# Kernel tuning notes

Measured on AMD Instinct MI355X. Metric: run time of the kernel, lower is better.

Reference implementation:

```python
import jax, jax.numpy as jnp
import numpy as np

H = 64  # hidden_size
IN = 1  # input_size
OUT = 32  # fc output


def _lstm_layer(x, Wih, Whh, bih, bhh):
    """x: (B,T,D_in). Returns (outputs (B,T,H), final h (B,H)). PyTorch gate order i,f,g,o."""
    B = x.shape[0]
    b = bih + bhh  # (4H,)
    # precompute input contributions for all timesteps: (T,B,4H)
    xW = jnp.einsum('btd,gd->tbg', x, Wih) + b

    def step(carry, xw_t):
        h, c = carry
        gates = xw_t + h @ Whh.T  # (B,4H)
        i, f, g, o = jnp.split(gates, 4, axis=-1)
        i = jax.nn.sigmoid(i)
        f = jax.nn.sigmoid(f)
        g = jnp.tanh(g)
        o = jax.nn.sigmoid(o)
        c = f * c + i * g
        h = o * jnp.tanh(c)
        return (h, c), h

    h0 = jnp.zeros((B, H), dtype=x.dtype)
    c0 = jnp.zeros((B, H), dtype=x.dtype)
    (h_T, _), hs = jax.lax.scan(step, (h0, c0), xW)
    return jnp.swapaxes(hs, 0, 1), h_T


def setup_inputs() -> dict:
    key = jax.random.key(0)
    ks = jax.random.split(key, 11)
    s_ih0 = 1.0 / np.sqrt(H)
    inp = {
        'x': jax.random.normal(ks[0], (2048, 512, IN), dtype=jnp.float32),
        # layer 0: input_size -> H
        'Wih0': jax.random.uniform(ks[1], (4 * H, IN), minval=-s_ih0, maxval=s_ih0),
        'Whh0': jax.random.uniform(ks[2], (4 * H, H), minval=-s_ih0, maxval=s_ih0),
        'bih0': jax.random.uniform(ks[3], (4 * H,), minval=-s_ih0, maxval=s_ih0),
        'bhh0': jax.random.uniform(ks[4], (4 * H,), minval=-s_ih0, maxval=s_ih0),
        # layer 1: H -> H
        'Wih1': jax.random.uniform(ks[5], (4 * H, H), minval=-s_ih0, maxval=s_ih0),
        'Whh1': jax.random.uniform(ks[6], (4 * H, H), minval=-s_ih0, maxval=s_ih0),
        'bih1': jax.random.uniform(ks[7], (4 * H,), minval=-s_ih0, maxval=s_ih0),
        'bhh1': jax.random.uniform(ks[8], (4 * H,), minval=-s_ih0, maxval=s_ih0),
        # fc: H -> 32
        'fcW': jax.random.uniform(ks[9], (OUT, H), minval=-s_ih0, maxval=s_ih0),
        'fcb': jax.random.uniform(ks[10], (OUT,), minval=-s_ih0, maxval=s_ih0),
    }
    return inp


def reference(x, Wih0, Whh0, bih0, bhh0, Wih1, Whh1, bih1, bhh1, fcW, fcb):
    h1_seq, _ = _lstm_layer(x, Wih0, Whh0, bih0, bhh0)
    _, h_last = _lstm_layer(h1_seq, Wih1, Whh1, bih1, bhh1)  # hidden[-1]
    features = jax.nn.relu(h_last @ fcW.T + fcb)  # (B, 32)
    return features
```

## Files before the change

### kernel.cpp

```cpp
#include <hip/hip_runtime.h>
#include <hip/hip_bf16.h>


#define HID 64
#define TSTEPS 512
#define MB 8
#define RS 80

typedef _Float16 f16x8 __attribute__((ext_vector_type(8)));
typedef float f32x4 __attribute__((ext_vector_type(4)));

#define KSIG (-1.44269504089f)
#define KTANH (2.88539008178f)

__device__ __forceinline__ float sig1(float p) {
    return __builtin_amdgcn_rcpf(1.f + __builtin_amdgcn_exp2f(p));
}
__device__ __forceinline__ float th1(float p) {
    return 1.f - 2.f * __builtin_amdgcn_rcpf(1.f + __builtin_amdgcn_exp2f(p));
}

#define MFMA16(A, B, C) __builtin_amdgcn_mfma_f32_16x16x32_f16((A), (B), (C), 0, 0, 0)

__global__ __launch_bounds__(512, 1) void lstm_feat_kernel(
    const float* __restrict__ x,
    const float* __restrict__ Wih0, const float* __restrict__ Whh0,
    const float* __restrict__ bih0, const float* __restrict__ bhh0,
    const float* __restrict__ Wih1, const float* __restrict__ Whh1,
    const float* __restrict__ bih1, const float* __restrict__ bhh1,
    const float* __restrict__ fcW, const float* __restrict__ fcb,
    float* __restrict__ out)
{
    __shared__ __align__(16) float x_lds[(MB / 2) * TSTEPS * 2];
    __shared__ __align__(16) _Float16 h0_lds[4][MB * RS];
    __shared__ __align__(16) _Float16 h1_lds[2][MB * RS];
    __shared__ float h1f32[MB * HID];
    __shared__ float fcw_lds[HID * 32];
    __shared__ float fcb_lds[32];

    const int tid  = threadIdx.x;
    const int wave = tid >> 6;
    const int lane = tid & 63;
    const int nq   = lane & 15;
    const int quad = lane >> 4;
    const int bbase = blockIdx.x * MB;
    const bool isL1 = (wave >= 4);
    const int ug = wave & 3;
    const int u  = ug * 16 + nq;

    for (int i = tid; i < TSTEPS * MB; i += 512) {
        int r = i >> 9, t = i & (TSTEPS - 1);
        x_lds[(r >> 1) * (TSTEPS * 2) + t * 2 + (r & 1)] = x[(bbase + r) * TSTEPS + t];
    }
    for (int i = tid; i < 32 * HID; i += 512) {
        int o = i >> 6, kk = i & 63;
        fcw_lds[kk * 32 + o] = fcW[i];
    }
    if (tid < 32) fcb_lds[tid] = fcb[tid];
    for (int i = tid; i < 4 * MB * RS; i += 512) ((_Float16*)h0_lds)[i] = (_Float16)0.f;
    for (int i = tid; i < 2 * MB * RS; i += 512) ((_Float16*)h1_lds)[i] = (_Float16)0.f;

    f16x8 wA[4][2], wB[4][2];
    f32x4 cbias[4];
    float wx0s[4];
    {
        const float* Wa = isL1 ? Wih1 : Whh0;
        const float* bi = isL1 ? bih1 : bih0;
        const float* bh = isL1 ? bhh1 : bhh0;
        #pragma unroll
        for (int g = 0; g < 4; ++g) {
            const float sc = (g == 2) ? KTANH : KSIG;
            const int n = g * 64 + u;
            const float bs = (bi[n] + bh[n]) * sc;
            cbias[g] = (f32x4){bs, bs, bs, bs};
            wx0s[g] = Wih0[n] * sc;
            #pragma unroll
            for (int ks = 0; ks < 2; ++ks) {
                const int k0 = quad * 8 + ks * 32;
                f16x8 a;
                #pragma unroll
                for (int j = 0; j < 8; ++j)
                    a[j] = (_Float16)(Wa[n * HID + k0 + j] * sc);
                wA[g][ks] = a;
            }
        }
        if (isL1) {
            #pragma unroll
            for (int g = 0; g < 4; ++g) {
                const float sc = (g == 2) ? KTANH : KSIG;
                const int n = g * 64 + u;
                #pragma unroll
                for (int ks = 0; ks < 2; ++ks) {
                    const int k0 = quad * 8 + ks * 32;
                    f16x8 b;
                    #pragma unroll
                    for (int j = 0; j < 8; ++j)
                        b[j] = (_Float16)(Whh1[n * HID + k0 + j] * sc);
                    wB[g][ks] = b;
                }
            }
        }
    }

    const int arow = (nq >> 1) * RS + quad * 8;
    const int b0r  = (quad * 2) * RS;
    const int hbase = quad * 2;
    float c0 = 0.f, c1 = 0.f;
    f32x4 l0ac[4], l1ac[4];

    __syncthreads();

#define L0A(S) do {                                                               \
    f16x8 a0 = *(const f16x8*)&h0_lds[S][arow];                                   \
    f16x8 a1 = *(const f16x8*)&h0_lds[S][arow + 32];                              \
    __builtin_amdgcn_s_setprio(1);                                                \
    _Pragma("unroll")                                                             \
    for (int g = 0; g < 4; ++g) l0ac[g] = MFMA16(a0, wA[g][0], cbias[g]);         \
    _Pragma("unroll")                                                             \
    for (int g = 0; g < 4; ++g) l0ac[g] = MFMA16(a1, wA[g][1], l0ac[g]);          \
    __builtin_amdgcn_s_setprio(0);                                                \
} while (0)

#define L0B(Q, XA, XB) do {                                                       \
    float pi0 = fmaf((XA), wx0s[0], l0ac[0][0]), pi1 = fmaf((XB), wx0s[0], l0ac[0][2]); \
    float pf0 = fmaf((XA), wx0s[1], l0ac[1][0]), pf1 = fmaf((XB), wx0s[1], l0ac[1][2]); \
    float pg0 = fmaf((XA), wx0s[2], l0ac[2][0]), pg1 = fmaf((XB), wx0s[2], l0ac[2][2]); \
    float po0 = fmaf((XA), wx0s[3], l0ac[3][0]), po1 = fmaf((XB), wx0s[3], l0ac[3][2]); \
    float iv0 = sig1(pi0), iv1 = sig1(pi1), fv0 = sig1(pf0), fv1 = sig1(pf1);     \
    float gv0 = th1(pg0),  gv1 = th1(pg1),  ov0 = sig1(po0), ov1 = sig1(po1);     \
    c0 = fmaf(fv0, c0, iv0 * gv0);  c1 = fmaf(fv1, c1, iv1 * gv1);                \
    h0_lds[Q][b0r + u]      = (_Float16)(ov0 * th1(c0 * KTANH));                  \
    h0_lds[Q][b0r + RS + u] = (_Float16)(ov1 * th1(c1 * KTANH));                  \
} while (0)

#define L1A(H1S) do {                                                             \
    float iv0 = sig1(l1ac[0][0]), iv1 = sig1(l1ac[0][2]);                         \
    float fv0 = sig1(l1ac[1][0]), fv1 = sig1(l1ac[1][2]);                         \
    float gv0 = th1(l1ac[2][0]),  gv1 = th1(l1ac[2][2]);                          \
    float ov0 = sig1(l1ac[3][0]), ov1 = sig1(l1ac[3][2]);                         \
    c0 = fmaf(fv0, c0, iv0 * gv0);  c1 = fmaf(fv1, c1, iv1 * gv1);                \
    h1_lds[H1S][b0r + u]      = (_Float16)(ov0 * th1(c0 * KTANH));                \
    h1_lds[H1S][b0r + RS + u] = (_Float16)(ov1 * th1(c1 * KTANH));                \
} while (0)

#define L1B(SH0, H1S) do {                                                        \
    f16x8 a00 = *(const f16x8*)&h0_lds[SH0][arow];                                \
    f16x8 a01 = *(const f16x8*)&h0_lds[SH0][arow + 32];                           \
    f16x8 a10 = *(const f16x8*)&h1_lds[H1S][arow];                                \
    f16x8 a11 = *(const f16x8*)&h1_lds[H1S][arow + 32];                           \
    __builtin_amdgcn_s_setprio(1);                                                \
    _Pragma("unroll")                                                             \
    for (int g = 0; g < 4; ++g) l1ac[g] = MFMA16(a00, wA[g][0], cbias[g]);        \
    _Pragma("unroll")                                                             \
    for (int g = 0; g < 4; ++g) l1ac[g] = MFMA16(a01, wA[g][1], l1ac[g]);         \
    _Pragma("unroll")                                                             \
    for (int g = 0; g < 4; ++g) l1ac[g] = MFMA16(a10, wB[g][0], l1ac[g]);         \
    _Pragma("unroll")                                                             \
    for (int g = 0; g < 4; ++g) l1ac[g] = MFMA16(a11, wB[g][1], l1ac[g]);         \
    __builtin_amdgcn_s_setprio(0);                                                \
} while (0)

#define IV(S, H1S, XA, XB, DOA, DOB) do {                                         \
    if (!isL1) { L0A(S); } else if (DOA) { L1A(H1S); }                            \
    __syncthreads();                                                              \
    if (!isL1) { L0B((S + 1) & 3, XA, XB); } else if (DOB) { L1B((S + 3) & 3, H1S); } \
    __syncthreads();                                                              \
} while (0)

    const int xoff = quad * (TSTEPS * 2);

    {
        const f32x4 xv0 = *(const f32x4*)&x_lds[xoff + 0];
        const f32x4 xv1 = *(const f32x4*)&x_lds[xoff + 4];
        IV(0, 0, xv0[0], xv0[1], false, false);
        IV(1, 1, xv0[2], xv0[3], false, false);
        IV(2, 0, xv1[0], xv1[1], false, true);
        IV(3, 1, xv1[2], xv1[3], true,  true);
    }

    for (int n = 4; n < TSTEPS; n += 4) {
        const f32x4 xv0 = *(const f32x4*)&x_lds[xoff + n * 2];
        const f32x4 xv1 = *(const f32x4*)&x_lds[xoff + n * 2 + 4];
        IV(0, 0, xv0[0], xv0[1], true, true);
        IV(1, 1, xv0[2], xv0[3], true, true);
        IV(2, 0, xv1[0], xv1[1], true, true);
        IV(3, 1, xv1[2], xv1[3], true, true);
    }

    if (isL1) L1A(0);
    __syncthreads();
    if (isL1) L1B(3, 0);
    __syncthreads();
    if (isL1) L1A(1);
    __syncthreads();
    if (isL1) L1B(0, 1);
    __syncthreads();

    if (isL1) {
        float iv0 = sig1(l1ac[0][0]), iv1 = sig1(l1ac[0][2]);
        float fv0 = sig1(l1ac[1][0]), fv1 = sig1(l1ac[1][2]);
        float gv0 = th1(l1ac[2][0]),  gv1 = th1(l1ac[2][2]);
        float ov0 = sig1(l1ac[3][0]), ov1 = sig1(l1ac[3][2]);
        c0 = fmaf(fv0, c0, iv0 * gv0);  c1 = fmaf(fv1, c1, iv1 * gv1);
        h1f32[hbase * HID + u]       = ov0 * th1(c0 * KTANH);
        h1f32[(hbase + 1) * HID + u] = ov1 * th1(c1 * KTANH);
    }
    __syncthreads();

    if (tid < MB * 32) {
        const int o  = tid & 31;
        const int rr = tid >> 5;
        float acc = fcb_lds[o];
        #pragma unroll 8
        for (int kk = 0; kk < HID; ++kk)
            acc += h1f32[rr * HID + kk] * fcw_lds[kk * 32 + o];
        out[(bbase + rr) * 32 + o] = fmaxf(acc, 0.f);
    }
}

extern "C" void kernel_launch(void* const* d_in, const int* in_sizes, int n_in,
                              void* d_out, int out_size, void* d_ws, size_t ws_size,
                              hipStream_t stream) {
    const float* x    = (const float*)d_in[0];
    const float* Wih0 = (const float*)d_in[1];
    const float* Whh0 = (const float*)d_in[2];
    const float* bih0 = (const float*)d_in[3];
    const float* bhh0 = (const float*)d_in[4];
    const float* Wih1 = (const float*)d_in[5];
    const float* Whh1 = (const float*)d_in[6];
    const float* bih1 = (const float*)d_in[7];
    const float* bhh1 = (const float*)d_in[8];
    const float* fcW  = (const float*)d_in[9];
    const float* fcb  = (const float*)d_in[10];
    float* out = (float*)d_out;

    lstm_feat_kernel<<<2048 / MB, 512, 0, stream>>>(
        x, Wih0, Whh0, bih0, bhh0, Wih1, Whh1, bih1, bhh1, fcW, fcb, out);
}
```

Before: 337.8 us.

## Split LSTM gate work across 16 waves and pair gates via lane shuffles

The block grows from 512 to 1024 threads (16 waves). Each wave now covers 8 hidden units, with lanes 0-7 holding the i/g gates and lanes 8-15 holding f/o, and a shuffle xor 8 combines them for the cell update. This halves the MFMA chain and the transcendental work per wave on the serial recurrence. The 4-slot pipeline with two barriers per timestep becomes one barrier per step using double-buffered h. The x·Wih0 term moves into the MFMA accumulator init. The cost is twice as many waves competing for barriers and SIMDs, plus half the lanes idling during the stores.

New measurement: 373.3 us. +10.5%, slower.

```diff
diff --git a/kernel.cpp b/kernel.cpp
--- a/kernel.cpp
+++ b/kernel.cpp
@@ -13,16 +13,13 @@
 #define KSIG (-1.44269504089f)
 #define KTANH (2.88539008178f)
 
-__device__ __forceinline__ float sig1(float p) {
+__device__ __forceinline__ float rcp1p(float p) {
     return __builtin_amdgcn_rcpf(1.f + __builtin_amdgcn_exp2f(p));
 }
-__device__ __forceinline__ float th1(float p) {
-    return 1.f - 2.f * __builtin_amdgcn_rcpf(1.f + __builtin_amdgcn_exp2f(p));
-}
 
 #define MFMA16(A, B, C) __builtin_amdgcn_mfma_f32_16x16x32_f16((A), (B), (C), 0, 0, 0)
 
-__global__ __launch_bounds__(512, 1) void lstm_feat_kernel(
+__global__ __launch_bounds__(1024) void lstm_feat_kernel(
     const float* __restrict__ x,
     const float* __restrict__ Wih0, const float* __restrict__ Whh0,
     const float* __restrict__ bih0, const float* __restrict__ bhh0,
@@ -31,8 +28,8 @@
     const float* __restrict__ fcW, const float* __restrict__ fcb,
     float* __restrict__ out)
 {
-    __shared__ __align__(16) float x_lds[(MB / 2) * TSTEPS * 2];
-    __shared__ __align__(16) _Float16 h0_lds[4][MB * RS];
+    __shared__ __align__(16) float x_lds[4 * TSTEPS * 2];
+    __shared__ __align__(16) _Float16 h0_lds[2][MB * RS];
     __shared__ __align__(16) _Float16 h1_lds[2][MB * RS];
     __shared__ float h1f32[MB * HID];
     __shared__ float fcw_lds[HID * 32];
@@ -44,166 +41,177 @@
     const int nq   = lane & 15;
     const int quad = lane >> 4;
     const int bbase = blockIdx.x * MB;
-    const bool isL1 = (wave >= 4);
-    const int ug = wave & 3;
-    const int u  = ug * 16 + nq;
-
-    for (int i = tid; i < TSTEPS * MB; i += 512) {
+    const bool isL1 = (wave >= 8);
+    const int oct = (wave & 7) * 8;
+    const bool lo = (nq < 8);
+    const int uu = oct + (nq & 7);
+
+    for (int i = tid; i < TSTEPS * MB; i += 1024) {
         int r = i >> 9, t = i & (TSTEPS - 1);
         x_lds[(r >> 1) * (TSTEPS * 2) + t * 2 + (r & 1)] = x[(bbase + r) * TSTEPS + t];
     }
-    for (int i = tid; i < 32 * HID; i += 512) {
+    for (int i = tid; i < 32 * HID; i += 1024) {
         int o = i >> 6, kk = i & 63;
         fcw_lds[kk * 32 + o] = fcW[i];
     }
     if (tid < 32) fcb_lds[tid] = fcb[tid];
-    for (int i = tid; i < 4 * MB * RS; i += 512) ((_Float16*)h0_lds)[i] = (_Float16)0.f;
-    for (int i = tid; i < 2 * MB * RS; i += 512) ((_Float16*)h1_lds)[i] = (_Float16)0.f;
-
-    f16x8 wA[4][2], wB[4][2];
-    f32x4 cbias[4];
-    float wx0s[4];
-    {
-        const float* Wa = isL1 ? Wih1 : Whh0;
-        const float* bi = isL1 ? bih1 : bih0;
-        const float* bh = isL1 ? bhh1 : bhh0;
-        #pragma unroll
-        for (int g = 0; g < 4; ++g) {
-            const float sc = (g == 2) ? KTANH : KSIG;
-            const int n = g * 64 + u;
-            const float bs = (bi[n] + bh[n]) * sc;
-            cbias[g] = (f32x4){bs, bs, bs, bs};
-            wx0s[g] = Wih0[n] * sc;
+    for (int i = tid; i < 2 * MB * RS; i += 1024) {
+        ((_Float16*)h0_lds)[i] = (_Float16)0.f;
+        ((_Float16*)h1_lds)[i] = (_Float16)0.f;
+    }
+
+    int   ntab[2];
+    float scl[2];
+    #pragma unroll
+    for (int t = 0; t < 2; ++t) {
+        const int gate = 2 * t + (lo ? 0 : 1);
+        ntab[t] = gate * 64 + uu;
+        scl[t]  = (gate == 2) ? KTANH : KSIG;
+    }
+    const float selA = lo ? -2.f : 1.f;
+    const float selB = lo ?  1.f : 0.f;
+
+    f16x8 wf[2][4];
+    float wx0v[2], bsv[2];
+    f32x4 cbv[2];
+    if (!isL1) {
+        #pragma unroll
+        for (int t = 0; t < 2; ++t) {
+            const int n = ntab[t];
+            wx0v[t] = Wih0[n] * scl[t];
+            bsv[t]  = (bih0[n] + bhh0[n]) * scl[t];
             #pragma unroll
             for (int ks = 0; ks < 2; ++ks) {
-                const int k0 = quad * 8 + ks * 32;
                 f16x8 a;
                 #pragma unroll
                 for (int j = 0; j < 8; ++j)
-                    a[j] = (_Float16)(Wa[n * HID + k0 + j] * sc);
-                wA[g][ks] = a;
+                    a[j] = (_Float16)(Whh0[n * HID + quad * 8 + ks * 32 + j] * scl[t]);
+                wf[t][ks] = a;
             }
         }
-        if (isL1) {
+    } else {
+        #pragma unroll
+        for (int t = 0; t < 2; ++t) {
+            const int n = ntab[t];
+            const float cb = (bih1[n] + bhh1[n]) * scl[t];
+            cbv[t] = (f32x4){cb, cb, cb, cb};
             #pragma unroll
-            for (int g = 0; g < 4; ++g) {
-                const float sc = (g == 2) ? KTANH : KSIG;
-                const int n = g * 64 + u;
+            for (int ks = 0; ks < 4; ++ks) {
+                const float* W = (ks < 2) ? Wih1 : Whh1;
+                const int k0 = quad * 8 + (ks & 1) * 32;
+                f16x8 a;
                 #pragma unroll
-                for (int ks = 0; ks < 2; ++ks) {
-                    const int k0 = quad * 8 + ks * 32;
-                    f16x8 b;
-                    #pragma unroll
-                    for (int j = 0; j < 8; ++j)
-                        b[j] = (_Float16)(Whh1[n * HID + k0 + j] * sc);
-                    wB[g][ks] = b;
-                }
+                for (int j = 0; j < 8; ++j)
+                    a[j] = (_Float16)(W[n * HID + k0 + j] * scl[t]);
+                wf[t][ks] = a;
             }
         }
     }
 
     const int arow = (nq >> 1) * RS + quad * 8;
     const int b0r  = (quad * 2) * RS;
-    const int hbase = quad * 2;
     float c0 = 0.f, c1 = 0.f;
-    f32x4 l0ac[4], l1ac[4];
 
     __syncthreads();
 
-#define L0A(S) do {                                                               \
-    f16x8 a0 = *(const f16x8*)&h0_lds[S][arow];                                   \
-    f16x8 a1 = *(const f16x8*)&h0_lds[S][arow + 32];                              \
+#define CELL(A0, A1, DST, GUARD) do {                                             \
+    float r0a = rcp1p((A0)[0]), r0b = rcp1p((A0)[2]);                \
+    float r1a = rcp1p((A1)[0]), r1b = rcp1p((A1)[2]);                             \
+    float va = fmaf(selA, r1a, selB), vb = fmaf(selA, r1b, selB);    \
+    float sa = __shfl_xor(r0a * va, 8);               \
+    float sb = __shfl_xor(r0b * vb, 8);                                           \
+    if (GUARD) {                                                                  \
+        c0 = fmaf(r0a, c0, sa);  c1 = fmaf(r0b, c1, sb);                          \
+        float ha = va * (1.f - 2.f * rcp1p(c0 * KTANH));                          \
+        float hb = vb * (1.f - 2.f * rcp1p(c1 * KTANH));                          \
+        if (!lo) {                                                                \
+            (DST)[b0r + uu]      = (_Float16)ha;                                  \
+            (DST)[b0r + RS + uu] = (_Float16)hb;                                  \
+        }                                                                         \
+    }                                                                             \
+} while (0)
+
+#define L0_STEP(P, Q, XA, XB) do {                                                \
+    f16x8 a0 = *(const f16x8*)&h0_lds[P][arow];                                   \
+    f16x8 a1 = *(const f16x8*)&h0_lds[P][arow + 32];                              \
+    f32x4 A[2];                                                                   \
     __builtin_amdgcn_s_setprio(1);                                                \
     _Pragma("unroll")                                                             \
-    for (int g = 0; g < 4; ++g) l0ac[g] = MFMA16(a0, wA[g][0], cbias[g]);         \
-    _Pragma("unroll")                                                             \
-    for (int g = 0; g < 4; ++g) l0ac[g] = MFMA16(a1, wA[g][1], l0ac[g]);          \
+    for (int t = 0; t < 2; ++t) {                                                 \
+        f32x4 C;                                                                  \
+        C[0] = fmaf((XA), wx0v[t], bsv[t]); C[1] = 0.f;                           \
+        C[2] = fmaf((XB), wx0v[t], bsv[t]); C[3] = 0.f;                           \
+        A[t] = MFMA16(a0, wf[t][0], C);                                           \
+    }                                                                             \
+    _Pragma("unroll")                                                             \
+    for (int t = 0; t < 2; ++t) A[t] = MFMA16(a1, wf[t][1], A[t]);                \
     __builtin_amdgcn_s_setprio(0);                                                \
+    CELL(A[0], A[1], h0_lds[Q], true);                                            \
 } while (0)
 
-#define L0B(Q, XA, XB) do {                                                       \
-    float pi0 = fmaf((XA), wx0s[0], l0ac[0][0]), pi1 = fmaf((XB), wx0s[0], l0ac[0][2]); \
-    float pf0 = fmaf((XA), wx0s[1], l0ac[1][0]), pf1 = fmaf((XB), wx0s[1], l0ac[1][2]); \
-    float pg0 = fmaf((XA), wx0s[2], l0ac[2][0]), pg1 = fmaf((XB), wx0s[2], l0ac[2][2]); \
-    float po0 = fmaf((XA), wx0s[3], l0ac[3][0]), po1 = fmaf((XB), wx0s[3], l0ac[3][2]); \
-    float iv0 = sig1(pi0), iv1 = sig1(pi1), fv0 = sig1(pf0), fv1 = sig1(pf1);     \
-    float gv0 = th1(pg0),  gv1 = th1(pg1),  ov0 = sig1(po0), ov1 = sig1(po1);     \
-    c0 = fmaf(fv0, c0, iv0 * gv0);  c1 = fmaf(fv1, c1, iv1 * gv1);                \
-    h0_lds[Q][b0r + u]      = (_Float16)(ov0 * th1(c0 * KTANH));                  \
-    h0_lds[Q][b0r + RS + u] = (_Float16)(ov1 * th1(c1 * KTANH));                  \
+#define L1_STEP(P, Q, GUARD) do {                                                 \
+    f16x8 a0  = *(const f16x8*)&h0_lds[P][arow];                                  \
+    f16x8 a1  = *(const f16x8*)&h0_lds[P][arow + 32];                             \
+    f16x8 b0v = *(const f16x8*)&h1_lds[P][arow];                                  \
+    f16x8 b1v = *(const f16x8*)&h1_lds[P][arow + 32];                             \
+    f32x4 A[2];                                                                   \
+    __builtin_amdgcn_s_setprio(1);                                                \
+    _Pragma("unroll")                                                             \
+    for (int t = 0; t < 2; ++t) A[t] = MFMA16(a0, wf[t][0], cbv[t]);              \
+    _Pragma("unroll")                                                             \
+    for (int t = 0; t < 2; ++t) A[t] = MFMA16(a1, wf[t][1], A[t]);                \
+    _Pragma("unroll")                                                             \
+    for (int t = 0; t < 2; ++t) A[t] = MFMA16(b0v, wf[t][2], A[t]);               \
+    _Pragma("unroll")                                                             \
+    for (int t = 0; t < 2; ++t) A[t] = MFMA16(b1v, wf[t][3], A[t]);               \
+    __builtin_amdgcn_s_setprio(0);                                                \
+    CELL(A[0], A[1], h1_lds[Q], GUARD);                                           \
 } while (0)
 
-#define L1A(H1S) do {                                                             \
-    float iv0 = sig1(l1ac[0][0]), iv1 = sig1(l1ac[0][2]);                         \
-    float fv0 = sig1(l1ac[1][0]), fv1 = sig1(l1ac[1][2]);                         \
-    float gv0 = th1(l1ac[2][0]),  gv1 = th1(l1ac[2][2]);                          \
-    float ov0 = sig1(l1ac[3][0]), ov1 = sig1(l1ac[3][2]);                         \
-    c0 = fmaf(fv0, c0, iv0 * gv0);  c1 = fmaf(fv1, c1, iv1 * gv1);                \
-    h1_lds[H1S][b0r + u]      = (_Float16)(ov0 * th1(c0 * KTANH));                \
-    h1_lds[H1S][b0r + RS + u] = (_Float16)(ov1 * th1(c1 * KTANH));                \
-} while (0)
-
-#define L1B(SH0, H1S) do {                                                        \
-    f16x8 a00 = *(const f16x8*)&h0_lds[SH0][arow];                                \
-    f16x8 a01 = *(const f16x8*)&h0_lds[SH0][arow + 32];                           \
-    f16x8 a10 = *(const f16x8*)&h1_lds[H1S][arow];                                \
-    f16x8 a11 = *(const f16x8*)&h1_lds[H1S][arow + 32];                           \
-    __builtin_amdgcn_s_setprio(1);                                                \
-    _Pragma("unroll")                                                             \
-    for (int g = 0; g < 4; ++g) l1ac[g] = MFMA16(a00, wA[g][0], cbias[g]);        \
-    _Pragma("unroll")                                                             \
-    for (int g = 0; g < 4; ++g) l1ac[g] = MFMA16(a01, wA[g][1], l1ac[g]);         \
-    _Pragma("unroll")                                                             \
-    for (int g = 0; g < 4; ++g) l1ac[g] = MFMA16(a10, wB[g][0], l1ac[g]);         \
-    _Pragma("unroll")                                                             \
-    for (int g = 0; g < 4; ++g) l1ac[g] = MFMA16(a11, wB[g][1], l1ac[g]);         \
-    __builtin_amdgcn_s_setprio(0);                                                \
-} while (0)
-
-#define IV(S, H1S, XA, XB, DOA, DOB) do {                                         \
-    if (!isL1) { L0A(S); } else if (DOA) { L1A(H1S); }                            \
-    __syncthreads();                                                              \
-    if (!isL1) { L0B((S + 1) & 3, XA, XB); } else if (DOB) { L1B((S + 3) & 3, H1S); } \
-    __syncthreads();                                                              \
-} while (0)
-
     const int xoff = quad * (TSTEPS * 2);
 
     {
-        const f32x4 xv0 = *(const f32x4*)&x_lds[xoff + 0];
-        const f32x4 xv1 = *(const f32x4*)&x_lds[xoff + 4];
-        IV(0, 0, xv0[0], xv0[1], false, false);
-        IV(1, 1, xv0[2], xv0[3], false, false);
-        IV(2, 0, xv1[0], xv1[1], false, true);
-        IV(3, 1, xv1[2], xv1[3], true,  true);
-    }
-
-    for (int n = 4; n < TSTEPS; n += 4) {
-        const f32x4 xv0 = *(const f32x4*)&x_lds[xoff + n * 2];
-        const f32x4 xv1 = *(const f32x4*)&x_lds[xoff + n * 2 + 4];
-        IV(0, 0, xv0[0], xv0[1], true, true);
-        IV(1, 1, xv0[2], xv0[3], true, true);
-        IV(2, 0, xv1[0], xv1[1], true, true);
-        IV(3, 1, xv1[2], xv1[3], true, true);
-    }
-
-    if (isL1) L1A(0);
-    __syncthreads();
-    if (isL1) L1B(3, 0);
-    __syncthreads();
-    if (isL1) L1A(1);
-    __syncthreads();
-    if (isL1) L1B(0, 1);
-    __syncthreads();
+        const f32x4 xv = *(const f32x4*)&x_lds[xoff + 0];
+        if (!isL1) L0_STEP(0, 1, xv[0], xv[1]); else L1_STEP(0, 1, false);
+        __syncthreads();
+        if (!isL1) L0_STEP(1, 0, xv[2], xv[3]); else L1_STEP(1, 0, true);
+        __syncthreads();
+    }
+
+    for (int k = 2; k < TSTEPS; k += 2) {
+        const f32x4 xv = *(const f32x4*)&x_lds[xoff + k * 2];
+        if (!isL1) L0_STEP(0, 1, xv[0], xv[1]); else L1_STEP(0, 1, true);
+        __syncthreads();
+        if (!isL1) L0_STEP(1, 0, xv[2], xv[3]); else L1_STEP(1, 0, true);
+        __syncthreads();
+    }
 
     if (isL1) {
-        float iv0 = sig1(l1ac[0][0]), iv1 = sig1(l1ac[0][2]);
-        float fv0 = sig1(l1ac[1][0]), fv1 = sig1(l1ac[1][2]);
-        float gv0 = th1(l1ac[2][0]),  gv1 = th1(l1ac[2][2]);
-        float ov0 = sig1(l1ac[3][0]), ov1 = sig1(l1ac[3][2]);
-        c0 = fmaf(fv0, c0, iv0 * gv0);  c1 = fmaf(fv1, c1, iv1 * gv1);
-        h1f32[hbase * HID + u]       = ov0 * th1(c0 * KTANH);
-        h1f32[(hbase + 1) * HID + u] = ov1 * th1(c1 * KTANH);
+        f16x8 a0  = *(const f16x8*)&h0_lds[0][arow];
+        f16x8 a1  = *(const f16x8*)&h0_lds[0][arow + 32];
+        f16x8 b0v = *(const f16x8*)&h1_lds[0][arow];
+        f16x8 b1v = *(const f16x8*)&h1_lds[0][arow + 32];
+        f32x4 A[2];
+        #pragma unroll
+        for (int t = 0; t < 2; ++t) A[t] = MFMA16(a0, wf[t][0], cbv[t]);
+        #pragma unroll
+        for (int t = 0; t < 2; ++t) A[t] = MFMA16(a1, wf[t][1], A[t]);
+        #pragma unroll
+        for (int t = 0; t < 2; ++t) A[t] = MFMA16(b0v, wf[t][2], A[t]);
+        #pragma unroll
+        for (int t = 0; t < 2; ++t) A[t] = MFMA16(b1v, wf[t][3], A[t]);
+        float r0a = rcp1p(A[0][0]), r0b = rcp1p(A[0][2]);
+        float r1a = rcp1p(A[1][0]), r1b = rcp1p(A[1][2]);
+        float va = fmaf(selA, r1a, selB), vb = fmaf(selA, r1b, selB);
+        float sa = __shfl_xor(r0a * va, 8);
+        float sb = __shfl_xor(r0b * vb, 8);
+        c0 = fmaf(r0a, c0, sa);  c1 = fmaf(r0b, c1, sb);
+        float ha = va * (1.f - 2.f * rcp1p(c0 * KTANH));
+        float hb = vb * (1.f - 2.f * rcp1p(c1 * KTANH));
+        if (!lo) {
+            h1f32[(quad * 2) * HID + uu]     = ha;
+            h1f32[(quad * 2 + 1) * HID + uu] = hb;
+        }
     }
     __syncthreads();
 
@@ -234,6 +242,6 @@
     const float* fcb  = (const float*)d_in[10];
     float* out = (float*)d_out;
 
-    lstm_feat_kernel<<<2048 / MB, 512, 0, stream>>>(
+    lstm_feat_kernel<<<2048 / MB, 1024, 0, stream>>>(
         x, Wih0, Whh0, bih0, bhh0, Wih1, Whh1, bih1, bhh1, fcW, fcb, out);
 }
```

## Split LSTM gate columns across all waves, running both layers per wave with one barrier

Applied to the files above, without the earlier changes.

Previously four waves ran layer 0 and four ran layer 1, with two barriers per step. Now every one of the eight waves owns an 8-unit slice of both layers: it computes layer-0 and layer-1 MFMAs for its columns in the same step, then exchanges gate values with lane shuffles so each lane holds all four gates for one (batch, unit) pair. This halves the barriers per step and balances the work across waves. It also folds the x*Wih0 term and the bias into the MFMA accumulator init. The cost is three weight sets held in registers per wave, plus extra shuffles and selects.

Result: slower. 370.9 us (+9.8%).

```diff
diff --git a/kernel.cpp b/kernel.cpp
--- a/kernel.cpp
+++ b/kernel.cpp
@@ -13,11 +13,8 @@
 #define KSIG (-1.44269504089f)
 #define KTANH (2.88539008178f)
 
-__device__ __forceinline__ float sig1(float p) {
+__device__ __forceinline__ float rcp1p(float p) {
     return __builtin_amdgcn_rcpf(1.f + __builtin_amdgcn_exp2f(p));
-}
-__device__ __forceinline__ float th1(float p) {
-    return 1.f - 2.f * __builtin_amdgcn_rcpf(1.f + __builtin_amdgcn_exp2f(p));
 }
 
 #define MFMA16(A, B, C) __builtin_amdgcn_mfma_f32_16x16x32_f16((A), (B), (C), 0, 0, 0)
@@ -31,7 +28,7 @@
     const float* __restrict__ fcW, const float* __restrict__ fcb,
     float* __restrict__ out)
 {
-    __shared__ __align__(16) float x_lds[(MB / 2) * TSTEPS * 2];
+    __shared__ __align__(16) float x_lds[4 * TSTEPS * 2];
     __shared__ __align__(16) _Float16 h0_lds[4][MB * RS];
     __shared__ __align__(16) _Float16 h1_lds[2][MB * RS];
     __shared__ float h1f32[MB * HID];
@@ -43,10 +40,9 @@
     const int lane = tid & 63;
     const int nq   = lane & 15;
     const int quad = lane >> 4;
+    const int oct  = wave * 8;
+    const bool lo  = (nq < 8);
     const int bbase = blockIdx.x * MB;
-    const bool isL1 = (wave >= 4);
-    const int ug = wave & 3;
-    const int u  = ug * 16 + nq;
 
     for (int i = tid; i < TSTEPS * MB; i += 512) {
         int r = i >> 9, t = i & (TSTEPS - 1);
@@ -60,110 +56,103 @@
     for (int i = tid; i < 4 * MB * RS; i += 512) ((_Float16*)h0_lds)[i] = (_Float16)0.f;
     for (int i = tid; i < 2 * MB * RS; i += 512) ((_Float16*)h1_lds)[i] = (_Float16)0.f;
 
-    f16x8 wA[4][2], wB[4][2];
-    f32x4 cbias[4];
-    float wx0s[4];
-    {
-        const float* Wa = isL1 ? Wih1 : Whh0;
-        const float* bi = isL1 ? bih1 : bih0;
-        const float* bh = isL1 ? bhh1 : bhh0;
+    f16x8 w0[2][2], wi1[2][2], wh1[2][2];
+    float bs0[2], wx0[2];
+    f32x4 cb1[2];
+    #pragma unroll
+    for (int t = 0; t < 2; ++t) {
+        const int gate = 2 * t + (nq >> 3);
+        const int n = gate * 64 + oct + (nq & 7);
+        const float sc = (gate == 2) ? KTANH : KSIG;
+        bs0[t] = (bih0[n] + bhh0[n]) * sc;
+        wx0[t] = Wih0[n] * sc;
+        const float cb = (bih1[n] + bhh1[n]) * sc;
+        cb1[t] = (f32x4){cb, cb, cb, cb};
         #pragma unroll
-        for (int g = 0; g < 4; ++g) {
-            const float sc = (g == 2) ? KTANH : KSIG;
-            const int n = g * 64 + u;
-            const float bs = (bi[n] + bh[n]) * sc;
-            cbias[g] = (f32x4){bs, bs, bs, bs};
-            wx0s[g] = Wih0[n] * sc;
+        for (int ks = 0; ks < 2; ++ks) {
+            const int k0 = quad * 8 + ks * 32;
+            f16x8 a, b, c;
             #pragma unroll
-            for (int ks = 0; ks < 2; ++ks) {
-                const int k0 = quad * 8 + ks * 32;
-                f16x8 a;
-                #pragma unroll
-                for (int j = 0; j < 8; ++j)
-                    a[j] = (_Float16)(Wa[n * HID + k0 + j] * sc);
-                wA[g][ks] = a;
+            for (int j = 0; j < 8; ++j) {
+                a[j] = (_Float16)(Whh0[n * HID + k0 + j] * sc);
+                b[j] = (_Float16)(Wih1[n * HID + k0 + j] * sc);
+                c[j] = (_Float16)(Whh1[n * HID + k0 + j] * sc);
             }
+            w0[t][ks] = a; wi1[t][ks] = b; wh1[t][ks] = c;
         }
-        if (isL1) {
-            #pragma unroll
-            for (int g = 0; g < 4; ++g) {
-                const float sc = (g == 2) ? KTANH : KSIG;
-                const int n = g * 64 + u;
-                #pragma unroll
-                for (int ks = 0; ks < 2; ++ks) {
-                    const int k0 = quad * 8 + ks * 32;
-                    f16x8 b;
-                    #pragma unroll
-                    for (int j = 0; j < 8; ++j)
-                        b[j] = (_Float16)(Whh1[n * HID + k0 + j] * sc);
-                    wB[g][ks] = b;
-                }
-            }
-        }
     }
 
     const int arow = (nq >> 1) * RS + quad * 8;
-    const int b0r  = (quad * 2) * RS;
-    const int hbase = quad * 2;
-    float c0 = 0.f, c1 = 0.f;
-    f32x4 l0ac[4], l1ac[4];
+    const int wrow = (quad * 2 + (lo ? 0 : 1)) * RS + oct + (nq & 7);
+    const int wfc  = (quad * 2 + (lo ? 0 : 1)) * HID + oct + (nq & 7);
+    float cl0 = 0.f, cl1 = 0.f;
 
     __syncthreads();
 
-#define L0A(S) do {                                                               \
-    f16x8 a0 = *(const f16x8*)&h0_lds[S][arow];                                   \
-    f16x8 a1 = *(const f16x8*)&h0_lds[S][arow + 32];                              \
+#define L0_MM(SR, X0, X1, OUT) do {                                               \
+    f16x8 a0 = *(const f16x8*)&h0_lds[SR][arow];                                  \
+    f16x8 a1 = *(const f16x8*)&h0_lds[SR][arow + 32];                             \
+    _Pragma("unroll")                                                             \
+    for (int t = 0; t < 2; ++t) {                                                 \
+        const float c0v = fmaf((X0), wx0[t], bs0[t]);                             \
+        const float c1v = fmaf((X1), wx0[t], bs0[t]);                             \
+        f32x4 C = {c0v, c0v, c1v, c1v};                                           \
+        OUT[t] = MFMA16(a0, w0[t][0], C);                                         \
+    }                                                                             \
+    _Pragma("unroll")                                                             \
+    for (int t = 0; t < 2; ++t) OUT[t] = MFMA16(a1, w0[t][1], OUT[t]);            \
+} while (0)
+
+#define L1_MM(S0, S1, OUT) do {                                                   \
+    f16x8 p0 = *(const f16x8*)&h0_lds[S0][arow];                                  \
+    f16x8 p1 = *(const f16x8*)&h0_lds[S0][arow + 32];                             \
+    f16x8 q0 = *(const f16x8*)&h1_lds[S1][arow];                                  \
+    f16x8 q1 = *(const f16x8*)&h1_lds[S1][arow + 32];                             \
+    _Pragma("unroll")                                                             \
+    for (int t = 0; t < 2; ++t) OUT[t] = MFMA16(p0, wi1[t][0], cb1[t]);           \
+    _Pragma("unroll")                                                             \
+    for (int t = 0; t < 2; ++t) OUT[t] = MFMA16(p1, wi1[t][1], OUT[t]);           \
+    _Pragma("unroll")                                                             \
+    for (int t = 0; t < 2; ++t) OUT[t] = MFMA16(q0, wh1[t][0], OUT[t]);           \
+    _Pragma("unroll")                                                             \
+    for (int t = 0; t < 2; ++t) OUT[t] = MFMA16(q1, wh1[t][1], OUT[t]);           \
+} while (0)
+
+#define CELLX(AC, CST, HOUT) do {                                                 \
+    float r1 = __shfl_xor(lo ? AC[0][2] : AC[0][0], 8);                           \
+    float r2 = __shfl_xor(lo ? AC[1][2] : AC[1][0], 8);                           \
+    float pi = lo ? AC[0][0] : r1;                                                \
+    float pf = lo ? r1 : AC[0][2];                                                \
+    float pg = lo ? AC[1][0] : r2;                                                \
+    float po = lo ? r2 : AC[1][2];                                                \
+    float iv = rcp1p(pi), fv = rcp1p(pf), ov = rcp1p(po);                         \
+    float gv = 1.f - 2.f * rcp1p(pg);                                             \
+    CST = fmaf(fv, CST, iv * gv);                                                 \
+    HOUT = ov * (1.f - 2.f * rcp1p(CST * KTANH));                                 \
+} while (0)
+
+#define IV_FULL(NM4, X0, X1) do {                                                 \
+    f32x4 A0[2], A1[2];                                                           \
     __builtin_amdgcn_s_setprio(1);                                                \
-    _Pragma("unroll")                                                             \
-    for (int g = 0; g < 4; ++g) l0ac[g] = MFMA16(a0, wA[g][0], cbias[g]);         \
-    _Pragma("unroll")                                                             \
-    for (int g = 0; g < 4; ++g) l0ac[g] = MFMA16(a1, wA[g][1], l0ac[g]);          \
+    L0_MM((NM4) & 3, X0, X1, A0);                                                 \
+    L1_MM(((NM4) + 3) & 3, (NM4) & 1, A1);                                        \
     __builtin_amdgcn_s_setprio(0);                                                \
-} while (0)
-
-#define L0B(Q, XA, XB) do {                                                       \
-    float pi0 = fmaf((XA), wx0s[0], l0ac[0][0]), pi1 = fmaf((XB), wx0s[0], l0ac[0][2]); \
-    float pf0 = fmaf((XA), wx0s[1], l0ac[1][0]), pf1 = fmaf((XB), wx0s[1], l0ac[1][2]); \
-    float pg0 = fmaf((XA), wx0s[2], l0ac[2][0]), pg1 = fmaf((XB), wx0s[2], l0ac[2][2]); \
-    float po0 = fmaf((XA), wx0s[3], l0ac[3][0]), po1 = fmaf((XB), wx0s[3], l0ac[3][2]); \
-    float iv0 = sig1(pi0), iv1 = sig1(pi1), fv0 = sig1(pf0), fv1 = sig1(pf1);     \
-    float gv0 = th1(pg0),  gv1 = th1(pg1),  ov0 = sig1(po0), ov1 = sig1(po1);     \
-    c0 = fmaf(fv0, c0, iv0 * gv0);  c1 = fmaf(fv1, c1, iv1 * gv1);                \
-    h0_lds[Q][b0r + u]      = (_Float16)(ov0 * th1(c0 * KTANH));                  \
-    h0_lds[Q][b0r + RS + u] = (_Float16)(ov1 * th1(c1 * KTANH));                  \
-} while (0)
-
-#define L1A(H1S) do {                                                             \
-    float iv0 = sig1(l1ac[0][0]), iv1 = sig1(l1ac[0][2]);                         \
-    float fv0 = sig1(l1ac[1][0]), fv1 = sig1(l1ac[1][2]);                         \
-    float gv0 = th1(l1ac[2][0]),  gv1 = th1(l1ac[2][2]);                          \
-    float ov0 = sig1(l1ac[3][0]), ov1 = sig1(l1ac[3][2]);                         \
-    c0 = fmaf(fv0, c0, iv0 * gv0);  c1 = fmaf(fv1, c1, iv1 * gv1);                \
-    h1_lds[H1S][b0r + u]      = (_Float16)(ov0 * th1(c0 * KTANH));                \
-    h1_lds[H1S][b0r + RS + u] = (_Float16)(ov1 * th1(c1 * KTANH));                \
-} while (0)
-
-#define L1B(SH0, H1S) do {                                                        \
-    f16x8 a00 = *(const f16x8*)&h0_lds[SH0][arow];                                \
-    f16x8 a01 = *(const f16x8*)&h0_lds[SH0][arow + 32];                           \
-    f16x8 a10 = *(const f16x8*)&h1_lds[H1S][arow];                                \
-    f16x8 a11 = *(const f16x8*)&h1_lds[H1S][arow + 32];                           \
+    float h0v, h1v;                                                               \
+    CELLX(A0, cl0, h0v);                                                          \
+    h0_lds[((NM4) + 1) & 3][wrow] = (_Float16)h0v;                                \
+    CELLX(A1, cl1, h1v);                                                          \
+    h1_lds[((NM4) + 1) & 1][wrow] = (_Float16)h1v;                                \
+    __syncthreads();                                                              \
+} while (0)
+
+#define IV_L0(NM4, X0, X1) do {                                                   \
+    f32x4 A0[2];                                                                  \
     __builtin_amdgcn_s_setprio(1);                                                \
-    _Pragma("unroll")                                                             \
-    for (int g = 0; g < 4; ++g) l1ac[g] = MFMA16(a00, wA[g][0], cbias[g]);        \
-    _Pragma("unroll")                                                             \
-    for (int g = 0; g < 4; ++g) l1ac[g] = MFMA16(a01, wA[g][1], l1ac[g]);         \
-    _Pragma("unroll")                                                             \
-    for (int g = 0; g < 4; ++g) l1ac[g] = MFMA16(a10, wB[g][0], l1ac[g]);         \
-    _Pragma("unroll")                                                             \
-    for (int g = 0; g < 4; ++g) l1ac[g] = MFMA16(a11, wB[g][1], l1ac[g]);         \
+    L0_MM((NM4) & 3, X0, X1, A0);                                                 \
     __builtin_amdgcn_s_setprio(0);                                                \
-} while (0)
-
-#define IV(S, H1S, XA, XB, DOA, DOB) do {                                         \
-    if (!isL1) { L0A(S); } else if (DOA) { L1A(H1S); }                            \
-    __syncthreads();                                                              \
-    if (!isL1) { L0B((S + 1) & 3, XA, XB); } else if (DOB) { L1B((S + 3) & 3, H1S); } \
+    float h0v;                                                                    \
+    CELLX(A0, cl0, h0v);                                                          \
+    h0_lds[((NM4) + 1) & 3][wrow] = (_Float16)h0v;                                \
     __syncthreads();                                                              \
 } while (0)
 
@@ -172,38 +161,35 @@
     {
         const f32x4 xv0 = *(const f32x4*)&x_lds[xoff + 0];
         const f32x4 xv1 = *(const f32x4*)&x_lds[xoff + 4];
-        IV(0, 0, xv0[0], xv0[1], false, false);
-        IV(1, 1, xv0[2], xv0[3], false, false);
-        IV(2, 0, xv1[0], xv1[1], false, true);
-        IV(3, 1, xv1[2], xv1[3], true,  true);
+        IV_L0(0, xv0[0], xv0[1]);
+        IV_L0(1, xv0[2], xv0[3]);
+        IV_FULL(2, xv1[0], xv1[1]);
+        IV_FULL(3, xv1[2], xv1[3]);
     }
 
     for (int n = 4; n < TSTEPS; n += 4) {
         const f32x4 xv0 = *(const f32x4*)&x_lds[xoff + n * 2];
         const f32x4 xv1 = *(const f32x4*)&x_lds[xoff + n * 2 + 4];
-        IV(0, 0, xv0[0], xv0[1], true, true);
-        IV(1, 1, xv0[2], xv0[3], true, true);
-        IV(2, 0, xv1[0], xv1[1], true, true);
-        IV(3, 1, xv1[2], xv1[3], true, true);
-    }
-
-    if (isL1) L1A(0);
+        IV_FULL(0, xv0[0], xv0[1]);
+        IV_FULL(1, xv0[2], xv0[3]);
+        IV_FULL(2, xv1[0], xv1[1]);
+        IV_FULL(3, xv1[2], xv1[3]);
+    }
+
+    {
+        f32x4 A1[2];
+        L1_MM(3, 0, A1);
+        float h1v;
+        CELLX(A1, cl1, h1v);
+        h1_lds[1][wrow] = (_Float16)h1v;
+    }
     __syncthreads();
-    if (isL1) L1B(3, 0);
-    __syncthreads();
-    if (isL1) L1A(1);
-    __syncthreads();
-    if (isL1) L1B(0, 1);
-    __syncthreads();
-
-    if (isL1) {
-        float iv0 = sig1(l1ac[0][0]), iv1 = sig1(l1ac[0][2]);
-        float fv0 = sig1(l1ac[1][0]), fv1 = sig1(l1ac[1][2]);
-        float gv0 = th1(l1ac[2][0]),  gv1 = th1(l1ac[2][2]);
-        float ov0 = sig1(l1ac[3][0]), ov1 = sig1(l1ac[3][2]);
-        c0 = fmaf(fv0, c0, iv0 * gv0);  c1 = fmaf(fv1, c1, iv1 * gv1);
-        h1f32[hbase * HID + u]       = ov0 * th1(c0 * KTANH);
-        h1f32[(hbase + 1) * HID + u] = ov1 * th1(c1 * KTANH);
+    {
+        f32x4 A1[2];
+        L1_MM(0, 1, A1);
+        float h1v;
+        CELLX(A1, cl1, h1v);
+        h1f32[wfc] = h1v;
     }
     __syncthreads();
 
```
